# Performance work log

Hardware: AMD Instinct MI355X
Metric: run time of the kernel (lower is better)

The kernel has to match this reference:

```python
import jax, jax.numpy as jnp
import numpy as np

NUM_D = 48          # num_depth_dense
MIN_D, MAX_D = 1.0, 60.0
IOU_T = 0.05
SR_MIN, SR_MAX = -51.2, 51.2
MAXQ = 400          # max_queries
IMG_AREA_HI = 800 * 448 * 0.55
NEG_INF = -jnp.inf


def setup_inputs() -> dict:
    key = jax.random.key(0)
    k1, k2, k3, k4 = jax.random.split(key, 4)
    B, NC, N = 8, 6, 900
    x1 = jax.random.uniform(k1, (B, NC, N), minval=0.0, maxval=700.0)
    y1 = jax.random.uniform(k2, (B, NC, N), minval=0.0, maxval=350.0)
    w = jax.random.uniform(k3, (B, NC, N), minval=5.0, maxval=160.0)
    h = jax.random.uniform(k4, (B, NC, N), minval=5.0, maxval=110.0)
    boxes_2d = jnp.stack([x1, y1, x1 + w, y1 + h], axis=-1)

    rng = np.random.default_rng(0)
    K = np.tile(np.eye(4, dtype=np.float32), (B, NC, 1, 1))
    f = (500.0 * (1.0 + 0.1 * rng.random((B, NC)))).astype(np.float32)
    K[..., 0, 0] = f; K[..., 1, 1] = f
    K[..., 0, 2] = 400.0; K[..., 1, 2] = 224.0

    th = rng.uniform(-np.pi, np.pi, (B, NC))
    ph = rng.uniform(-0.1, 0.1, (B, NC))
    c, s = np.cos(th), np.sin(th)
    cp, sp = np.cos(ph), np.sin(ph)
    Rz = np.zeros((B, NC, 3, 3)); Rz[..., 0, 0] = c; Rz[..., 0, 1] = -s; Rz[..., 1, 0] = s; Rz[..., 1, 1] = c; Rz[..., 2, 2] = 1.0
    Rx = np.zeros((B, NC, 3, 3)); Rx[..., 0, 0] = 1.0; Rx[..., 1, 1] = cp; Rx[..., 1, 2] = -sp; Rx[..., 2, 1] = sp; Rx[..., 2, 2] = cp
    E = np.tile(np.eye(4, dtype=np.float32), (B, NC, 1, 1))
    E[..., :3, :3] = (Rz @ Rx).astype(np.float32)
    E[..., :3, 3] = rng.uniform(-2.0, 2.0, (B, NC, 3)).astype(np.float32)

    return {
        'boxes_2d': boxes_2d,
        'cam_intrinsics': jnp.asarray(K),
        'cam_extrinsics': jnp.asarray(E.astype(np.float32)),
        'depth_std_base': jnp.ones((1,), dtype=jnp.float32),
    }


def _nan_to_num(x):
    return jnp.nan_to_num(x, nan=0.0, posinf=1e6, neginf=-1e6)


def _iou(b1, b2):
    x1 = jnp.maximum(b1[..., 0], b2[..., 0])
    y1 = jnp.maximum(b1[..., 1], b2[..., 1])
    x2 = jnp.minimum(b1[..., 2], b2[..., 2])
    y2 = jnp.minimum(b1[..., 3], b2[..., 3])
    inter = jnp.clip(x2 - x1, 0.0) * jnp.clip(y2 - y1, 0.0)
    a1 = (b1[..., 2] - b1[..., 0]) * (b1[..., 3] - b1[..., 1])
    a2 = (b2[..., 2] - b2[..., 0]) * (b2[..., 3] - b2[..., 1])
    return inter / (a1 + a2 - inter + 1e-6)


def _forward(boxes_2d, K, E, depth_std_base):
    # boxes_2d: [B,NC,N,4], K/E: [B,NC,4,4]
    B, NC, N, _ = boxes_2d.shape
    D = NUM_D
    centers = jnp.stack([(boxes_2d[..., 0] + boxes_2d[..., 2]) * 0.5,
                         (boxes_2d[..., 1] + boxes_2d[..., 3]) * 0.5], axis=-1)  # [B,NC,N,2]
    depths = jnp.broadcast_to(jnp.linspace(MIN_D, MAX_D, D, dtype=boxes_2d.dtype),
                              (B, NC, N, D))

    # ---- back-projection: pixel (u,v,d) -> camera -> ego ----
    pts2d = centers[..., None, :] * depths[..., None]                 # [B,NC,N,D,2]
    p_cam = jnp.concatenate([pts2d, depths[..., None]], axis=-1)      # [B,NC,N,D,3]
    Kinv = _nan_to_num(jnp.linalg.inv(K[..., :3, :3]))
    p_cam = jnp.einsum('bcij,bcndj->bcndi', Kinv, p_cam)
    p_hom = jnp.concatenate([p_cam, jnp.ones_like(p_cam[..., :1])], axis=-1)
    points_3d = jnp.einsum('bcij,bcndj->bcndi', E, p_hom)[..., :3]    # [B,NC,N,D,3]

    # ---- projection consistency filter ----
    areas = (boxes_2d[..., 2] - boxes_2d[..., 0]) * (boxes_2d[..., 3] - boxes_2d[..., 1])
    valid_box = (areas > 5.0) & (areas < IMG_AREA_HI)                 # [B,NC,N]
    p3h = jnp.concatenate([points_3d, jnp.ones_like(points_3d[..., :1])], axis=-1)
    Einv = _nan_to_num(jnp.linalg.inv(E))
    pch = jnp.einsum('bcij,bcndj->bcndi', Einv, p3h)
    pc = pch[..., :3] / (pch[..., 3:4] + 1e-6)
    pih = jnp.einsum('bcij,bcndj->bcndi', K[..., :3, :3], pc)
    img = pih[..., :2] / (pih[..., 2:3] + 1e-6)
    depth_scale = pc[..., 2:3]
    box_size = jnp.clip(40.0 * (10.0 / (depth_scale + 1e-6)), 8.0, 200.0)
    pseudo = jnp.concatenate([img - box_size / 2, img + box_size / 2], axis=-1)
    iou = _iou(pseudo, boxes_2d[..., None, :])                        # [B,NC,N,D]
    final_mask = (iou > IOU_T) & valid_box[..., None]                 # [B,NC,N,D]

    # ---- fixed-shape per-batch selection (pad to MAXQ) ----
    M = NC * N * D
    pts = points_3d.reshape(B, M, 3)
    msk = final_mask.reshape(B, M)
    area_f = jnp.broadcast_to(areas[..., None], (B, NC, N, D)).reshape(B, M)
    count = msk.sum(axis=-1)                                          # [B]
    key_area = jnp.where(msk, area_f, NEG_INF)
    key_order = jnp.where(msk, -jnp.arange(M, dtype=pts.dtype), NEG_INF)
    # match torch: original order when count<=MAXQ, else topk by area
    key = jnp.where((count > MAXQ)[:, None], key_area, key_order)
    vals, idx = jax.lax.top_k(key, MAXQ)                              # [B,MAXQ]
    sel = jnp.take_along_axis(pts, idx[..., None], axis=1)            # [B,MAXQ,3]
    pad_mask = ~jnp.isfinite(vals)
    sel = jnp.where(pad_mask[..., None], 0.0, sel)
    ref = jnp.clip((sel - SR_MIN) / (SR_MAX - SR_MIN + 1e-6), 0.0, 1.0)
    return ref, pad_mask


def reference(boxes_2d, cam_intrinsics, cam_extrinsics, depth_std_base):
    return _forward(boxes_2d, cam_intrinsics, cam_extrinsics, depth_std_base)
```

## Files before the change

### kernel.cpp

```cpp
#include <hip/hip_runtime.h>
#include <math.h>
#include <stdint.h>

#define BB 8
#define NCC 6
#define NBOX 900
#define NBOXES (NCC * NBOX)
#define NBC (BB * NCC)
#define ND 48
#define TPB_BOX 6
#define NQ 400
#define REFSZ (BB * NQ * 3)
#define NPAD 5408

__device__ __forceinline__ float nnf(double x) {
    float v = (float)x;
    if (isnan(v)) return 0.0f;
    if (isinf(v)) return v > 0.0f ? 1e6f : -1e6f;
    return v;
}

__device__ void invert3x3(const float* __restrict__ Kp, float* __restrict__ Ki) {
    double a00 = Kp[0], a01 = Kp[1], a02 = Kp[2];
    double a10 = Kp[4], a11 = Kp[5], a12 = Kp[6];
    double a20 = Kp[8], a21 = Kp[9], a22 = Kp[10];
    double c00 = a11 * a22 - a12 * a21;
    double c10 = a12 * a20 - a10 * a22;
    double c20 = a10 * a21 - a11 * a20;
    double det = a00 * c00 + a01 * c10 + a02 * c20;
    double id  = 1.0 / det;
    Ki[0] = nnf(c00 * id); Ki[1] = nnf((a02 * a21 - a01 * a22) * id); Ki[2] = nnf((a01 * a12 - a02 * a11) * id);
    Ki[3] = nnf(c10 * id); Ki[4] = nnf((a00 * a22 - a02 * a20) * id); Ki[5] = nnf((a02 * a10 - a00 * a12) * id);
    Ki[6] = nnf(c20 * id); Ki[7] = nnf((a01 * a20 - a00 * a21) * id); Ki[8] = nnf((a00 * a11 - a01 * a10) * id);
}

__device__ void invert4x4(const float* __restrict__ Ep, float* __restrict__ Ei) {
    double m[4][8];
    for (int i = 0; i < 4; ++i)
        for (int j = 0; j < 4; ++j) {
            m[i][j]     = (double)Ep[i * 4 + j];
            m[i][4 + j] = (i == j) ? 1.0 : 0.0;
        }
    for (int col = 0; col < 4; ++col) {
        int piv = col; double best = fabs(m[col][col]);
        for (int r = col + 1; r < 4; ++r) {
            double v = fabs(m[r][col]);
            if (v > best) { best = v; piv = r; }
        }
        if (piv != col)
            for (int j = 0; j < 8; ++j) { double tmp = m[col][j]; m[col][j] = m[piv][j]; m[piv][j] = tmp; }
        double ipv = 1.0 / m[col][col];
        for (int j = 0; j < 8; ++j) m[col][j] *= ipv;
        for (int r = 0; r < 4; ++r) {
            if (r == col) continue;
            double f = m[r][col];
            if (f != 0.0)
                for (int j = 0; j < 8; ++j) m[r][j] -= f * m[col][j];
        }
    }
    for (int i = 0; i < 16; ++i) Ei[i] = nnf(m[i / 4][4 + (i & 3)]);
}

__global__ __launch_bounds__(256) void mask_kernel(const float* __restrict__ boxes,
                                                   const float* __restrict__ K,
                                                   const float* __restrict__ E,
                                                   uint8_t* __restrict__ mask_bytes,
                                                   uint32_t* __restrict__ area_bits) {
    __shared__ float sKi[2][9];
    __shared__ float sEv[2][16];

    int gbase = blockIdx.x * 256;
    int bc_lo = gbase / (NBOX * TPB_BOX);
    int bc_hi = (gbase + 255) / (NBOX * TPB_BOX);
    if (bc_hi > NBC - 1) bc_hi = NBC - 1;
    if (threadIdx.x == 0) {
        invert3x3(K + bc_lo * 16, sKi[0]);
        invert4x4(E + bc_lo * 16, sEv[0]);
    }
    if (threadIdx.x == 1 && bc_hi != bc_lo) {
        invert3x3(K + bc_hi * 16, sKi[1]);
        invert4x4(E + bc_hi * 16, sEv[1]);
    }
    __syncthreads();

    int gtid = gbase + threadIdx.x;
    if (gtid >= BB * NBOXES * TPB_BOX) return;
    int box = gtid / TPB_BOX;
    int j   = gtid - box * TPB_BOX;
    int bc  = box / NBOX;

    const float* bx = boxes + box * 4;
    float x1 = bx[0], y1 = bx[1], x2 = bx[2], y2 = bx[3];
    float area  = (x2 - x1) * (y2 - y1);
    bool  valid = (area > 5.0f) && (area < 197120.0f);
    if (j == 0) {
        area_bits[box] = __float_as_uint(area);
        *(uint16_t*)(mask_bytes + box * 8 + 6) = 0;
    }

    uint32_t m8 = 0;
    if (valid) {
        int sel = (bc == bc_lo) ? 0 : 1;
        float Ki[9], Ev[16], Ep[12], Kp[11];
        #pragma unroll
        for (int i = 0; i < 9; ++i)  Ki[i] = sKi[sel][i];
        #pragma unroll
        for (int i = 0; i < 16; ++i) Ev[i] = sEv[sel][i];
        const float* Epp = E + bc * 16;
        #pragma unroll
        for (int i = 0; i < 12; ++i) Ep[i] = Epp[i];
        const float* Kpp = K + bc * 16;
        #pragma unroll
        for (int i = 0; i < 11; ++i) Kp[i] = Kpp[i];

        float cx = (x1 + x2) * 0.5f, cy = (y1 + y2) * 0.5f;
        const float step = (60.0f - 1.0f) / 47.0f;

        #pragma unroll
        for (int dd = 0; dd < 8; ++dd) {
            int d = j * 8 + dd;
            float z = (d == ND - 1) ? 60.0f : 1.0f + (float)d * step;
            float u0 = cx * z, u1 = cy * z;
            float pcx = Ki[0] * u0 + Ki[1] * u1 + Ki[2] * z;
            float pcy = Ki[3] * u0 + Ki[4] * u1 + Ki[5] * z;
            float pcz = Ki[6] * u0 + Ki[7] * u1 + Ki[8] * z;

            float X = Ep[0] * pcx + Ep[1] * pcy + Ep[2]  * pcz + Ep[3];
            float Y = Ep[4] * pcx + Ep[5] * pcy + Ep[6]  * pcz + Ep[7];
            float Z = Ep[8] * pcx + Ep[9] * pcy + Ep[10] * pcz + Ep[11];

            float q0 = Ev[0]  * X + Ev[1]  * Y + Ev[2]  * Z + Ev[3];
            float q1 = Ev[4]  * X + Ev[5]  * Y + Ev[6]  * Z + Ev[7];
            float q2 = Ev[8]  * X + Ev[9]  * Y + Ev[10] * Z + Ev[11];
            float q3 = Ev[12] * X + Ev[13] * Y + Ev[14] * Z + Ev[15];
            float w  = q3 + 1e-6f;
            float r0 = q0 / w, r1 = q1 / w, r2 = q2 / w;

            float p0 = Kp[0] * r0 + Kp[1] * r1 + Kp[2]  * r2;
            float p1 = Kp[4] * r0 + Kp[5] * r1 + Kp[6]  * r2;
            float p2 = Kp[8] * r0 + Kp[9] * r1 + Kp[10] * r2;
            float iz = p2 + 1e-6f;
            float ix = p0 / iz, iy = p1 / iz;

            float bs = 40.0f * (10.0f / (r2 + 1e-6f));
            bs = fminf(fmaxf(bs, 8.0f), 200.0f);
            float hh = bs / 2.0f;
            float px1 = ix - hh, py1 = iy - hh, px2 = ix + hh, py2 = iy + hh;

            float ix1 = fmaxf(px1, x1), iy1 = fmaxf(py1, y1);
            float ix2 = fminf(px2, x2), iy2 = fminf(py2, y2);
            float inter = fmaxf(ix2 - ix1, 0.0f) * fmaxf(iy2 - iy1, 0.0f);
            float a1 = (px2 - px1) * (py2 - py1);
            float iou = inter / (a1 + area - inter + 1e-6f);

            if (iou > 0.05f) m8 |= (1u << dd);
        }
    }
    mask_bytes[box * 8 + j] = (uint8_t)m8;
}

__global__ __launch_bounds__(512) void select_kernel(const uint64_t* __restrict__ mask64,
                                                     const uint32_t* __restrict__ area_bits,
                                                     const float* __restrict__ boxes,
                                                     const float* __restrict__ K,
                                                     const float* __restrict__ E,
                                                     float* __restrict__ out) {
    int b   = blockIdx.x;
    int tid = threadIdx.x;
    const uint64_t* mb = mask64 + b * NBOXES;
    const uint32_t* ab = area_bits + b * NBOXES;

    __shared__ uint64_t s_key[NPAD];
    __shared__ uint64_t s_sel[512];
    __shared__ int      s_out[NQ];
    __shared__ int      s_hist[256];
    __shared__ int      s_scan[512];
    __shared__ float    s_Ki[NCC][9];
    __shared__ uint64_t s_prefix;
    __shared__ int      s_need, s_done, s_cnt;

    if (tid < NCC) invert3x3(K + (b * NCC + tid) * 16, s_Ki[tid]);
    if (tid < NQ) s_out[tid] = -1;

    int partial = 0;
    for (int t = tid; t < NPAD; t += 512) {
        uint64_t key = 0;
        if (t < NBOXES) {
            uint64_t mk = mb[t];
            int cnt = __popcll(mk);
            partial += cnt;
            if (cnt) key = ((uint64_t)ab[t] << 32) |
                           ((uint64_t)(NPAD - 1 - t) << 6) | (uint64_t)cnt;
        }
        s_key[t] = key;
    }
    s_scan[tid] = partial;
    __syncthreads();
    for (int s = 256; s > 0; s >>= 1) {
        if (tid < s) s_scan[tid] += s_scan[tid + s];
        __syncthreads();
    }
    int total = s_scan[0];
    __syncthreads();

    if (total > NQ) {
        if (tid == 0) { s_prefix = 0ull; s_need = NQ; s_done = 0; }
        __syncthreads();
        for (int shift = 56; shift >= 0; shift -= 8) {
            if (tid < 256) s_hist[tid] = 0;
            __syncthreads();
            uint64_t pref = s_prefix;
            for (int t = tid; t < NBOXES; t += 512) {
                uint64_t k = s_key[t];
                if (!k) continue;
                if (shift == 56 || (k >> (shift + 8)) == (pref >> (shift + 8)))
                    atomicAdd(&s_hist[(int)((k >> shift) & 255ull)], (int)(k & 63ull));
            }
            __syncthreads();
            if (tid < 64) {
                int h0 = s_hist[4 * tid + 0], h1 = s_hist[4 * tid + 1];
                int h2 = s_hist[4 * tid + 2], h3 = s_hist[4 * tid + 3];
                int lanesum = h0 + h1 + h2 + h3;
                int sufinc = lanesum;
                #pragma unroll
                for (int off = 1; off < 64; off <<= 1) {
                    int v = __shfl_down(sufinc, off);
                    if (tid + off < 64) sufinc += v;
                }
                int above = sufinc - lanesum;
                int need  = s_need;
                int C3 = above + h3;
                int C2 = C3 + h2;
                int C1 = C2 + h1;
                int C0 = C1 + h0;
                int dg = -1, hc = 0, Cnext = 0;
                if (C3 >= need && above < need) { dg = 4 * tid + 3; hc = h3; Cnext = above; }
                else if (C2 >= need && C3 < need) { dg = 4 * tid + 2; hc = h2; Cnext = C3; }
                else if (C1 >= need && C2 < need) { dg = 4 * tid + 1; hc = h1; Cnext = C2; }
                else if (C0 >= need && C1 < need) { dg = 4 * tid + 0; hc = h0; Cnext = C1; }
                if (dg >= 0) {
                    s_prefix = pref | ((uint64_t)dg << shift);
                    s_need   = need - Cnext;
                    if (hc == need - Cnext) s_done = 1;
                }
            }
            __syncthreads();
            if (s_done) break;
        }
        uint64_t T = s_prefix;

        if (tid == 0) s_cnt = 0;
        __syncthreads();
        for (int t = tid; t < NBOXES; t += 512) {
            uint64_t k = s_key[t];
            if (k && k >= T) {
                int p = atomicAdd(&s_cnt, 1);
                if (p < 512) s_sel[p] = k;
            }
        }
        __syncthreads();
        int C = s_cnt;
        if (C > 512) C = 512;

        if (tid < C) {
            uint64_t k = s_sel[tid];
            int w = (int)(k & 63ull);
            int start = 0;
            for (int j = 0; j < C; ++j) {
                uint64_t kj = s_sel[j];
                if (kj > k) start += (int)(kj & 63ull);
            }
            int cn = (NPAD - 1) - (int)((k >> 6) & 8191ull);
            uint64_t mask = mb[cn];
            for (int i = 0; i < w; ++i) {
                int d = __builtin_ctzll(mask);
                mask &= (mask - 1);
                int pos = start + i;
                if (pos < NQ) s_out[pos] = (cn << 6) | d;
            }
        }
        __syncthreads();
    } else {
        int base = tid * 11;
        int run = 0;
        for (int u = 0; u < 11; ++u) {
            int t = base + u;
            if (t < NBOXES) run += (int)(s_key[t] & 63ull);
        }
        s_scan[tid] = run;
        __syncthreads();
        for (int off = 1; off < 512; off <<= 1) {
            int v = (tid >= off) ? s_scan[tid - off] : 0;
            __syncthreads();
            s_scan[tid] += v;
            __syncthreads();
        }
        int pos = s_scan[tid] - run;
        for (int u = 0; u < 11; ++u) {
            int t = base + u;
            if (t >= NBOXES) break;
            uint64_t k = s_key[t];
            if (!k) continue;
            int w = (int)(k & 63ull);
            uint64_t mask = mb[t];
            for (int i = 0; i < w; ++i) {
                int d = __builtin_ctzll(mask);
                mask &= (mask - 1);
                if (pos < NQ) s_out[pos] = (t << 6) | d;
                ++pos;
            }
        }
        __syncthreads();
    }

    const float denom = 102.4f + 1e-6f;
    if (tid < NQ) {
        int v = s_out[tid];
        float X = 0.0f, Y = 0.0f, Z = 0.0f, pm = 1.0f;
        if (v >= 0) {
            int cn = v >> 6;
            int d  = v & 63;
            int c  = cn / NBOX;
            const float* bx = boxes + (b * NBOXES + cn) * 4;
            float x1 = bx[0], y1 = bx[1], x2 = bx[2], y2 = bx[3];
            float cx = (x1 + x2) * 0.5f, cy = (y1 + y2) * 0.5f;
            const float step = (60.0f - 1.0f) / 47.0f;
            float z = (d == ND - 1) ? 60.0f : 1.0f + (float)d * step;
            const float* Ki = s_Ki[c];
            float u0 = cx * z, u1 = cy * z;
            float pcx = Ki[0] * u0 + Ki[1] * u1 + Ki[2] * z;
            float pcy = Ki[3] * u0 + Ki[4] * u1 + Ki[5] * z;
            float pcz = Ki[6] * u0 + Ki[7] * u1 + Ki[8] * z;
            const float* Ep = E + (b * NCC + c) * 16;
            X = Ep[0] * pcx + Ep[1] * pcy + Ep[2]  * pcz + Ep[3];
            Y = Ep[4] * pcx + Ep[5] * pcy + Ep[6]  * pcz + Ep[7];
            Z = Ep[8] * pcx + Ep[9] * pcy + Ep[10] * pcz + Ep[11];
            pm = 0.0f;
        }
        float* o = out + (b * NQ + tid) * 3;
        o[0] = fminf(fmaxf((X + 51.2f) / denom, 0.0f), 1.0f);
        o[1] = fminf(fmaxf((Y + 51.2f) / denom, 0.0f), 1.0f);
        o[2] = fminf(fmaxf((Z + 51.2f) / denom, 0.0f), 1.0f);
        out[REFSZ + b * NQ + tid] = pm;
    }
}

extern "C" void kernel_launch(void* const* d_in, const int* in_sizes, int n_in,
                              void* d_out, int out_size, void* d_ws, size_t ws_size,
                              hipStream_t stream) {
    const float* boxes = (const float*)d_in[0];
    const float* K     = (const float*)d_in[1];
    const float* E     = (const float*)d_in[2];
    uint64_t* mask64    = (uint64_t*)d_ws;
    uint32_t* area_bits = (uint32_t*)((char*)d_ws + 345600);
    float*    out       = (float*)d_out;

    int nthreads = BB * NBOXES * TPB_BOX;
    mask_kernel<<<(nthreads + 255) / 256, 256, 0, stream>>>(
        boxes, K, E, (uint8_t*)mask64, area_bits);
    select_kernel<<<BB, 512, 0, stream>>>(mask64, area_bits, boxes, K, E, out);
}
```

Baseline: 105.9 us.

## Build area histogram in mask kernel to replace multi-pass radix select

The mask kernel now accumulates a per-batch 1024-bin histogram of masked depth counts keyed on the high bits of the box area, using global atomics. The select kernel reads this histogram, finds the threshold bin with one scan, and gathers candidates at or above it directly, replacing the shared-memory key array and the iterative 8-bit radix passes. It adds a memset launch and global atomic contention in the mask kernel. Correctness relies on the candidate set fitting within SELCAP; if the threshold bin is crowded, overflow candidates are dropped.

```diff
diff --git a/kernel.cpp b/kernel.cpp
--- a/kernel.cpp
+++ b/kernel.cpp
@@ -12,6 +12,8 @@
 #define NQ 400
 #define REFSZ (BB * NQ * 3)
 #define NPAD 5408
+#define NBIN 1024
+#define SELCAP 640
 
 __device__ __forceinline__ float nnf(double x) {
     float v = (float)x;
@@ -65,7 +67,8 @@
                                                    const float* __restrict__ K,
                                                    const float* __restrict__ E,
                                                    uint8_t* __restrict__ mask_bytes,
-                                                   uint32_t* __restrict__ area_bits) {
+                                                   uint32_t* __restrict__ area_bits,
+                                                   int* __restrict__ hist) {
     __shared__ float sKi[2][9];
     __shared__ float sEv[2][16];
 
@@ -88,13 +91,15 @@
     int box = gtid / TPB_BOX;
     int j   = gtid - box * TPB_BOX;
     int bc  = box / NBOX;
+    int b   = box / NBOXES;
 
     const float* bx = boxes + box * 4;
     float x1 = bx[0], y1 = bx[1], x2 = bx[2], y2 = bx[3];
     float area  = (x2 - x1) * (y2 - y1);
     bool  valid = (area > 5.0f) && (area < 197120.0f);
+    uint32_t abv = __float_as_uint(area);
     if (j == 0) {
-        area_bits[box] = __float_as_uint(area);
+        area_bits[box] = abv;
         *(uint16_t*)(mask_bytes + box * 8 + 6) = 0;
     }
 
@@ -157,6 +162,10 @@
         }
     }
     mask_bytes[box * 8 + j] = (uint8_t)m8;
+    if (m8) {
+        int bin = (int)(abv >> 21) & (NBIN - 1);
+        atomicAdd(&hist[b * NBIN + bin], __popc(m8));
+    }
 }
 
 __global__ __launch_bounds__(512) void select_kernel(const uint64_t* __restrict__ mask64,
@@ -164,128 +173,102 @@
                                                      const float* __restrict__ boxes,
                                                      const float* __restrict__ K,
                                                      const float* __restrict__ E,
+                                                     const int* __restrict__ hist,
                                                      float* __restrict__ out) {
     int b   = blockIdx.x;
     int tid = threadIdx.x;
+    int lane = tid & 63, wv = tid >> 6;
     const uint64_t* mb = mask64 + b * NBOXES;
     const uint32_t* ab = area_bits + b * NBOXES;
-
-    __shared__ uint64_t s_key[NPAD];
-    __shared__ uint64_t s_sel[512];
+    const int* hb = hist + b * NBIN;
+
+    __shared__ uint64_t s_sel[SELCAP];
     __shared__ int      s_out[NQ];
-    __shared__ int      s_hist[256];
     __shared__ int      s_scan[512];
+    __shared__ int      s_wsum[8];
     __shared__ float    s_Ki[NCC][9];
-    __shared__ uint64_t s_prefix;
-    __shared__ int      s_need, s_done, s_cnt;
+    __shared__ int      s_B, s_cnt;
 
     if (tid < NCC) invert3x3(K + (b * NCC + tid) * 16, s_Ki[tid]);
     if (tid < NQ) s_out[tid] = -1;
-
-    int partial = 0;
-    for (int t = tid; t < NPAD; t += 512) {
-        uint64_t key = 0;
-        if (t < NBOXES) {
+    if (tid == 0) { s_B = 0; s_cnt = 0; }
+
+    int h0 = hb[2 * tid];
+    int h1 = hb[2 * tid + 1];
+    int w  = h0 + h1;
+    int suf = w;
+    #pragma unroll
+    for (int off = 1; off < 64; off <<= 1) {
+        int v = __shfl_down(suf, off);
+        if (lane + off < 64) suf += v;
+    }
+    if (lane == 0) s_wsum[wv] = suf;
+    __syncthreads();
+    int above_waves = 0, total = 0;
+    #pragma unroll
+    for (int ww = 0; ww < 8; ++ww) {
+        int v = s_wsum[ww];
+        total += v;
+        if (ww > wv) above_waves += v;
+    }
+    int S_incl = suf + above_waves;
+    int above  = S_incl - w;
+    if (total > NQ) {
+        int s1 = above + h1;
+        if (s1 >= NQ && above < NQ)      s_B = 2 * tid + 1;
+        else if (S_incl >= NQ && s1 < NQ) s_B = 2 * tid;
+    }
+    __syncthreads();
+
+    if (total > NQ) {
+        int Bstar = s_B;
+        for (int t = tid; t < NBOXES; t += 512) {
             uint64_t mk = mb[t];
-            int cnt = __popcll(mk);
-            partial += cnt;
-            if (cnt) key = ((uint64_t)ab[t] << 32) |
-                           ((uint64_t)(NPAD - 1 - t) << 6) | (uint64_t)cnt;
-        }
-        s_key[t] = key;
-    }
-    s_scan[tid] = partial;
-    __syncthreads();
-    for (int s = 256; s > 0; s >>= 1) {
-        if (tid < s) s_scan[tid] += s_scan[tid + s];
-        __syncthreads();
-    }
-    int total = s_scan[0];
-    __syncthreads();
-
-    if (total > NQ) {
-        if (tid == 0) { s_prefix = 0ull; s_need = NQ; s_done = 0; }
-        __syncthreads();
-        for (int shift = 56; shift >= 0; shift -= 8) {
-            if (tid < 256) s_hist[tid] = 0;
-            __syncthreads();
-            uint64_t pref = s_prefix;
-            for (int t = tid; t < NBOXES; t += 512) {
-                uint64_t k = s_key[t];
-                if (!k) continue;
-                if (shift == 56 || (k >> (shift + 8)) == (pref >> (shift + 8)))
-                    atomicAdd(&s_hist[(int)((k >> shift) & 255ull)], (int)(k & 63ull));
-            }
-            __syncthreads();
-            if (tid < 64) {
-                int h0 = s_hist[4 * tid + 0], h1 = s_hist[4 * tid + 1];
-                int h2 = s_hist[4 * tid + 2], h3 = s_hist[4 * tid + 3];
-                int lanesum = h0 + h1 + h2 + h3;
-                int sufinc = lanesum;
-                #pragma unroll
-                for (int off = 1; off < 64; off <<= 1) {
-                    int v = __shfl_down(sufinc, off);
-                    if (tid + off < 64) sufinc += v;
-                }
-                int above = sufinc - lanesum;
-                int need  = s_need;
-                int C3 = above + h3;
-                int C2 = C3 + h2;
-                int C1 = C2 + h1;
-                int C0 = C1 + h0;
-                int dg = -1, hc = 0, Cnext = 0;
-                if (C3 >= need && above < need) { dg = 4 * tid + 3; hc = h3; Cnext = above; }
-                else if (C2 >= need && C3 < need) { dg = 4 * tid + 2; hc = h2; Cnext = C3; }
-                else if (C1 >= need && C2 < need) { dg = 4 * tid + 1; hc = h1; Cnext = C2; }
-                else if (C0 >= need && C1 < need) { dg = 4 * tid + 0; hc = h0; Cnext = C1; }
-                if (dg >= 0) {
-                    s_prefix = pref | ((uint64_t)dg << shift);
-                    s_need   = need - Cnext;
-                    if (hc == need - Cnext) s_done = 1;
-                }
-            }
-            __syncthreads();
-            if (s_done) break;
-        }
-        uint64_t T = s_prefix;
-
-        if (tid == 0) s_cnt = 0;
-        __syncthreads();
-        for (int t = tid; t < NBOXES; t += 512) {
-            uint64_t k = s_key[t];
-            if (k && k >= T) {
+            if (!mk) continue;
+            uint32_t abv = ab[t];
+            int bin = (int)(abv >> 21) & (NBIN - 1);
+            if (bin >= Bstar) {
                 int p = atomicAdd(&s_cnt, 1);
-                if (p < 512) s_sel[p] = k;
+                if (p < SELCAP)
+                    s_sel[p] = ((uint64_t)abv << 32) |
+                               ((uint64_t)(NPAD - 1 - t) << 6) |
+                               (uint64_t)__popcll(mk);
             }
         }
         __syncthreads();
         int C = s_cnt;
-        if (C > 512) C = 512;
-
-        if (tid < C) {
-            uint64_t k = s_sel[tid];
-            int w = (int)(k & 63ull);
+        if (C > SELCAP) C = SELCAP;
+
+        for (int i = tid; i < C; i += 512) {
+            uint64_t k = s_sel[i];
+            int wt = (int)(k & 63ull);
             int start = 0;
             for (int j = 0; j < C; ++j) {
                 uint64_t kj = s_sel[j];
                 if (kj > k) start += (int)(kj & 63ull);
             }
-            int cn = (NPAD - 1) - (int)((k >> 6) & 8191ull);
-            uint64_t mask = mb[cn];
-            for (int i = 0; i < w; ++i) {
-                int d = __builtin_ctzll(mask);
-                mask &= (mask - 1);
-                int pos = start + i;
-                if (pos < NQ) s_out[pos] = (cn << 6) | d;
+            if (start < NQ) {
+                int cn = (NPAD - 1) - (int)((k >> 6) & 8191ull);
+                uint64_t mask = mb[cn];
+                for (int u = 0; u < wt; ++u) {
+                    int d = __builtin_ctzll(mask);
+                    mask &= (mask - 1);
+                    int pos = start + u;
+                    if (pos < NQ) s_out[pos] = (cn << 6) | d;
+                }
             }
         }
         __syncthreads();
     } else {
         int base = tid * 11;
+        int cnts[11];
         int run = 0;
+        #pragma unroll
         for (int u = 0; u < 11; ++u) {
             int t = base + u;
-            if (t < NBOXES) run += (int)(s_key[t] & 63ull);
+            int c = (t < NBOXES) ? __popcll(mb[t]) : 0;
+            cnts[u] = c;
+            run += c;
         }
         s_scan[tid] = run;
         __syncthreads();
@@ -299,11 +282,10 @@
         for (int u = 0; u < 11; ++u) {
             int t = base + u;
             if (t >= NBOXES) break;
-            uint64_t k = s_key[t];
-            if (!k) continue;
-            int w = (int)(k & 63ull);
+            if (!cnts[u]) continue;
+            if (pos >= NQ) break;
             uint64_t mask = mb[t];
-            for (int i = 0; i < w; ++i) {
+            for (int i = 0; i < cnts[u]; ++i) {
                 int d = __builtin_ctzll(mask);
                 mask &= (mask - 1);
                 if (pos < NQ) s_out[pos] = (t << 6) | d;
@@ -353,10 +335,12 @@
     const float* E     = (const float*)d_in[2];
     uint64_t* mask64    = (uint64_t*)d_ws;
     uint32_t* area_bits = (uint32_t*)((char*)d_ws + 345600);
+    int*      histp     = (int*)((char*)d_ws + 518400);
     float*    out       = (float*)d_out;
 
+    hipMemsetAsync(histp, 0, BB * NBIN * sizeof(int), stream);
     int nthreads = BB * NBOXES * TPB_BOX;
     mask_kernel<<<(nthreads + 255) / 256, 256, 0, stream>>>(
-        boxes, K, E, (uint8_t*)mask64, area_bits);
-    select_kernel<<<BB, 512, 0, stream>>>(mask64, area_bits, boxes, K, E, out);
-}
+        boxes, K, E, (uint8_t*)mask64, area_bits, histp);
+    select_kernel<<<BB, 512, 0, stream>>>(mask64, area_bits, boxes, K, E, histp, out);
+}
```

Measured after the change: 274.1 us. +158.8%, slower.
